# Performance work log

Measured on AMD Instinct MI355X. Metric: run time of the kernel, lower is better.

## Reference

```python
import jax, jax.numpy as jnp
import numpy as np

HOP = 768
NCB = 14
DIM = 512
VOCAB = 1024
W_SCALE = 0.02  # keep conv stacks numerically tame


def conv1d(x, w, b, stride=1, padding=0):
    # x: [B,C,L], w: [O,I,K] (torch layout), b: [O]
    y = jax.lax.conv_general_dilated(
        x, w, window_strides=(stride,), padding=[(padding, padding)],
        dimension_numbers=('NCH', 'OIH', 'NCH'))
    return y + b[None, :, None]


def conv_transpose1d(x, w, b, stride, padding):
    # torch ConvTranspose1d weight layout: (in, out, k)
    k = w.shape[2]
    w2 = jnp.flip(jnp.transpose(w, (1, 0, 2)), axis=2)  # -> OIH
    y = jax.lax.conv_general_dilated(
        x, w2, window_strides=(1,),
        padding=[(k - 1 - padding, k - 1 - padding)],
        lhs_dilation=(stride,),
        dimension_numbers=('NCH', 'OIH', 'NCH'))
    return y + b[None, :, None]


def setup_inputs() -> dict:
    key = jax.random.key(0)
    ks = jax.random.split(key, 16)
    f = lambda k, shp, s=W_SCALE: jax.random.normal(k, shp, dtype=jnp.float32) * s
    B, T = 2, 98304  # T = 768 * 128
    return {
        'audio': jax.random.normal(ks[0], (B, 1, T), dtype=jnp.float32),
        'codebooks': jax.random.normal(ks[1], (NCB, VOCAB, DIM), dtype=jnp.float32),
        'ew1': f(ks[2], (256, 1, 7)), 'eb1': f(ks[3], (256,)),
        'ew2': f(ks[4], (512, 256, 5)), 'eb2': f(ks[5], (512,)),
        'ew3': f(ks[6], (NCB * DIM, 512, 3)), 'eb3': f(ks[7], (NCB * DIM,)),
        'dw1': f(ks[8], (NCB * DIM, 512, 5)), 'db1': f(ks[9], (512,)),
        'dw2': f(ks[10], (256, 512, 5)), 'db2': f(ks[11], (256,)),
        'dw3': f(ks[12], (1, 256, 7)), 'db3': f(ks[13], (1,)),
    }


def reference(audio, codebooks, ew1, eb1, ew2, eb2, ew3, eb3,
              dw1, db1, dw2, db2, dw3, db3):
    B = audio.shape[0]
    # ---- encoder ----
    h = jax.nn.relu(conv1d(audio, ew1, eb1, stride=1, padding=3))
    h = jax.nn.relu(conv1d(h, ew2, eb2, stride=HOP, padding=2))
    h = conv1d(h, ew3, eb3, stride=1, padding=1)          # [B, NCB*DIM, S]
    S = h.shape[-1]
    emb = h.reshape(B, NCB, DIM, S).transpose(0, 1, 3, 2)  # [B, NCB, S, DIM]
    # ---- VQ: per-codebook squared L2 distance + argmin (same argmin as cdist) ----
    d2 = (jnp.sum(emb * emb, axis=-1, keepdims=True)            # [B,NCB,S,1]
          - 2.0 * jnp.einsum('bksd,kvd->bksv', emb, codebooks)  # [B,NCB,S,V]
          + jnp.sum(codebooks * codebooks, axis=-1)[None, :, None, :])
    codes = jnp.argmin(d2, axis=-1)                        # [B, NCB, S] int
    # ---- decode: embedding lookup + transposed conv decoder ----
    q = codebooks[jnp.arange(NCB)[None, :, None], codes]   # [B, NCB, S, DIM]
    q = q.transpose(0, 1, 3, 2).reshape(B, NCB * DIM, S)   # [B, NCB*DIM, S]
    a = jax.nn.relu(conv_transpose1d(q, dw1, db1, stride=HOP, padding=2))
    a = jax.nn.relu(conv1d(a, dw2, db2, stride=1, padding=2))
    a = jnp.tanh(conv1d(a, dw3, db3, stride=1, padding=3))
    return a  # [B, 1, (S-1)*HOP + 1]
```

## Files before the change

### kernel.cpp

```cpp
#include <hip/hip_runtime.h>
#include <hip/hip_bf16.h>
#include <math.h>

#define T_IN 98304
#define SS 128
#define NBATCH 2
#define NN 256
#define C1 256
#define C2 512
#define C3 7168
#define NCBK 14
#define DIMV 512
#define VOC 1024
#define TOUT 97537
#define HOP 768

#define OFF_CBN    0L
#define OFF_AB1    14336L
#define OFF_AB2    14848L
#define OFF_CCONST 15104L
#define OFF_H2C    15120L
#define OFF_H2XH   146192L
#define OFF_H2XL   342800L
#define OFF_H3H    539408L
#define OFF_H3L    1456912L
#define OFF_SCORES 2374416L
#define OFF_X1H    2374416L
#define OFF_X1L    2538256L
#define OFF_DW1T   539408L
#define OFF_XH     539408L
#define OFF_XL     3488528L
#define OFF_CODES  9714448L
#define OFF_QBF    9718032L
#define OFF_A1RAW  10635536L
#define OFF_A2ACT  11290896L

typedef __attribute__((ext_vector_type(8))) short short8;
typedef __attribute__((ext_vector_type(4))) float f32x4;

static __device__ inline ushort f2bf(float x) {
  __hip_bfloat16 h = __float2bfloat16(x);
  return *reinterpret_cast<ushort*>(&h);
}

static __device__ inline void split8(const float4 x0, const float4 x1,
                                     short8& h, short8& l) {
  float xs[8] = {x0.x, x0.y, x0.z, x0.w, x1.x, x1.y, x1.z, x1.w};
  #pragma unroll
  for (int e = 0; e < 8; ++e) {
    uint b = __float_as_uint(xs[e]);
    h[e] = (short)(b >> 16);
    float r = xs[e] - __uint_as_float(b & 0xffff0000u);
    l[e] = (short)(__float_as_uint(r) >> 16);
  }
}

__global__ void k_cbn(const float* __restrict__ cb, float* __restrict__ cbn) {
  int row = blockIdx.x * 4 + (threadIdx.x >> 6);
  int lane = threadIdx.x & 63;
  const float* p = cb + (long)row * DIMV;
  float s = 0.f;
  for (int d = lane; d < DIMV; d += 64) { float x = p[d]; s += x * x; }
  for (int off = 32; off; off >>= 1) s += __shfl_down(s, off);
  if (lane == 0) cbn[row] = s;
}

__global__ __launch_bounds__(256) void k_prep_ab2(const float* __restrict__ db1,
    const float* __restrict__ dw2, const float* __restrict__ db2,
    float* __restrict__ ab1, float* __restrict__ ab2) {
  __shared__ float red[256];
  int o = blockIdx.x, t = threadIdx.x;
  if (o == 0) { ab1[t] = fmaxf(db1[t], 0.f); ab1[t + 256] = fmaxf(db1[t + 256], 0.f); }
  const float* wp = dw2 + (long)o * C2 * 5;
  float acc = 0.f;
  #pragma unroll
  for (int h = 0; h < 2; ++h) {
    int c = t + h * 256;
    const float* p = wp + c * 5;
    float wsum = p[0] + p[1] + p[2] + p[3] + p[4];
    acc = fmaf(wsum, fmaxf(db1[c], 0.f), acc);
  }
  red[t] = acc;
  __syncthreads();
  for (int off = 128; off; off >>= 1) {
    if (t < off) red[t] += red[t + off];
    __syncthreads();
  }
  if (t == 0) ab2[o] = fmaxf(red[0] + db2[o], 0.f);
}

__global__ __launch_bounds__(256) void k_prep_c(const float* __restrict__ dw3,
    const float* __restrict__ db3, const float* __restrict__ ab2,
    float* __restrict__ cconst) {
  __shared__ float red[256];
  int t = threadIdx.x;
  float wsum3 = 0.f;
  #pragma unroll
  for (int j = 0; j < 7; ++j) wsum3 += dw3[t*7+j];
  red[t] = wsum3 * ab2[t];
  __syncthreads();
  for (int off = 128; off; off >>= 1) {
    if (t < off) red[t] += red[t + off];
    __syncthreads();
  }
  if (t == 0) cconst[0] = tanhf(red[0] + db3[0]);
}

__global__ __launch_bounds__(256) void k_enc1(const float* __restrict__ audio,
    const float* __restrict__ ew1, const float* __restrict__ eb1,
    ushort* __restrict__ X1h, ushort* __restrict__ X1l) {
  int n = blockIdx.x, ic = threadIdx.x;
  int b = n >> 7, s = n & 127;
  const float* ap = audio + (long)b * T_IN;
  int base = HOP * s - 5;
  float a[11];
  #pragma unroll
  for (int w = 0; w < 11; ++w) {
    int ai = base + w;
    a[w] = (ai >= 0 && ai < T_IN) ? ap[ai] : 0.f;
  }
  float w1[7];
  #pragma unroll
  for (int j = 0; j < 7; ++j) w1[j] = ew1[ic*7+j];
  float b1 = eb1[ic];
  long off = (long)n * 1280 + ic * 5;
  #pragma unroll
  for (int jj = 0; jj < 5; ++jj) {
    int tcol = HOP * s + jj - 2;
    float v = 0.f;
    if (tcol >= 0) {
      float acc = b1;
      #pragma unroll
      for (int j = 0; j < 7; ++j) acc = fmaf(w1[j], a[jj + j], acc);
      v = fmaxf(acc, 0.f);
    }
    uint bi = __float_as_uint(v);
    X1h[off + jj] = (ushort)(bi >> 16);
    float r = v - __uint_as_float(bi & 0xffff0000u);
    X1l[off + jj] = (ushort)(__float_as_uint(r) >> 16);
  }
}

__global__ __launch_bounds__(256) void gemm_enc2(const float* __restrict__ ew2,
    const ushort* __restrict__ X1h, const ushort* __restrict__ X1l,
    const float* __restrict__ eb2, float* __restrict__ h2c) {
  __shared__ __align__(16) float red[4 * 2048];
  const int tid = threadIdx.x;
  const int w = tid >> 6, lane = tid & 63;
  const int l15 = lane & 15, quad = lane >> 4;
  const int m0 = blockIdx.x * 32, n0 = blockIdx.y * 64;
  const int kbase = w * 320;
  f32x4 acc[2][4] = {};
  const float*  aB = ew2 + (long)(m0 + l15) * 1280 + kbase + quad * 8;
  const ushort* bhB = X1h + (long)(n0 + l15) * 1280 + kbase + quad * 8;
  const ushort* blB = X1l + (long)(n0 + l15) * 1280 + kbase + quad * 8;
  for (int k0 = 0; k0 < 320; k0 += 32) {
    short8 ah[2], al[2], bh[4], bl[4];
    #pragma unroll
    for (int f = 0; f < 2; ++f) {
      const float* ap = aB + (long)f * 16 * 1280 + k0;
      float4 x0 = *(const float4*)ap;
      float4 x1 = *(const float4*)(ap + 4);
      split8(x0, x1, ah[f], al[f]);
    }
    #pragma unroll
    for (int f = 0; f < 4; ++f) {
      bh[f] = *(const short8*)(bhB + (long)f * 16 * 1280 + k0);
      bl[f] = *(const short8*)(blB + (long)f * 16 * 1280 + k0);
    }
    #pragma unroll
    for (int i = 0; i < 2; ++i)
      #pragma unroll
      for (int j = 0; j < 4; ++j) {
        acc[i][j] = __builtin_amdgcn_mfma_f32_16x16x32_bf16(ah[i], bh[j], acc[i][j], 0, 0, 0);
        acc[i][j] = __builtin_amdgcn_mfma_f32_16x16x32_bf16(ah[i], bl[j], acc[i][j], 0, 0, 0);
        acc[i][j] = __builtin_amdgcn_mfma_f32_16x16x32_bf16(al[i], bh[j], acc[i][j], 0, 0, 0);
      }
  }
  #pragma unroll
  for (int i = 0; i < 2; ++i)
    #pragma unroll
    for (int j = 0; j < 4; ++j)
      *(float4*)&red[w * 2048 + (i * 4 + j) * 256 + lane * 4] = *(float4*)&acc[i][j];
  __syncthreads();
  #pragma unroll
  for (int q = 0; q < 2; ++q) {
    const int c = 2 * w + q;
    const int i = c >> 2, j = c & 3;
    float4 s = make_float4(0.f, 0.f, 0.f, 0.f);
    #pragma unroll
    for (int g = 0; g < 4; ++g) {
      float4 t4 = *(const float4*)&red[g * 2048 + c * 256 + lane * 4];
      s.x += t4.x; s.y += t4.y; s.z += t4.z; s.w += t4.w;
    }
    const int obase = m0 + i * 16 + quad * 4;
    float4 bias = *(const float4*)(eb2 + obase);
    const int n = n0 + j * 16 + l15;
    float4 out;
    out.x = fmaxf(s.x + bias.x, 0.f);
    out.y = fmaxf(s.y + bias.y, 0.f);
    out.z = fmaxf(s.z + bias.z, 0.f);
    out.w = fmaxf(s.w + bias.w, 0.f);
    *(float4*)(h2c + (long)n * C2 + obase) = out;
  }
}

__global__ void k_h2x(const float* __restrict__ h2c, ushort* __restrict__ h2xh,
                      ushort* __restrict__ h2xl) {
  int idx = blockIdx.x * 256 + threadIdx.x;
  const int total = NN * 1536;
  for (; idx < total; idx += gridDim.x * 256) {
    int n = idx / 1536, r = idx - n * 1536;
    int ic = r / 3, j = r - ic * 3;
    int s2 = (n & 127) + j - 1;
    int b = n >> 7;
    float v = (s2 >= 0 && s2 < SS) ? h2c[(long)(b*SS + s2)*C2 + ic] : 0.f;
    uint bi = __float_as_uint(v);
    h2xh[idx] = (ushort)(bi >> 16);
    float rr = v - __uint_as_float(bi & 0xffff0000u);
    h2xl[idx] = (ushort)(__float_as_uint(rr) >> 16);
  }
}

__global__ __launch_bounds__(256) void gemm_h3(const float* __restrict__ A,
    const ushort* __restrict__ Bh, const ushort* __restrict__ Bl,
    const float* __restrict__ eb3, ushort* __restrict__ h3h, ushort* __restrict__ h3l) {
  __shared__ __align__(16) float red[4 * 4096];
  const int tid = threadIdx.x;
  const int w = tid >> 6, lane = tid & 63;
  const int l15 = lane & 15, quad = lane >> 4;
  const int m0 = blockIdx.x * 64, n0 = blockIdx.y * 64;
  const int kbase = w * 384;
  f32x4 acc[4][4] = {};
  const float*  aB = A  + (long)(m0 + l15) * 1536 + kbase + quad * 8;
  const ushort* bhB = Bh + (long)(n0 + l15) * 1536 + kbase + quad * 8;
  const ushort* blB = Bl + (long)(n0 + l15) * 1536 + kbase + quad * 8;
  for (int k0 = 0; k0 < 384; k0 += 32) {
    short8 ah[4], al[4], bh[4], bl[4];
    #pragma unroll
    for (int f = 0; f < 4; ++f) {
      const float* ap = aB + (long)f * 16 * 1536 + k0;
      float4 x0 = *(const float4*)ap;
      float4 x1 = *(const float4*)(ap + 4);
      split8(x0, x1, ah[f], al[f]);
      bh[f] = *(const short8*)(bhB + (long)f * 16 * 1536 + k0);
      bl[f] = *(const short8*)(blB + (long)f * 16 * 1536 + k0);
    }
    #pragma unroll
    for (int i = 0; i < 4; ++i)
      #pragma unroll
      for (int j = 0; j < 4; ++j) {
        acc[i][j] = __builtin_amdgcn_mfma_f32_16x16x32_bf16(ah[i], bh[j], acc[i][j], 0, 0, 0);
        acc[i][j] = __builtin_amdgcn_mfma_f32_16x16x32_bf16(ah[i], bl[j], acc[i][j], 0, 0, 0);
        acc[i][j] = __builtin_amdgcn_mfma_f32_16x16x32_bf16(al[i], bh[j], acc[i][j], 0, 0, 0);
      }
  }
  #pragma unroll
  for (int i = 0; i < 4; ++i)
    #pragma unroll
    for (int j = 0; j < 4; ++j)
      *(float4*)&red[w * 4096 + (i * 4 + j) * 256 + lane * 4] = *(float4*)&acc[i][j];
  __syncthreads();
  const int mbase = m0 + w * 16 + quad * 4;
  float4 bias = *(const float4*)(eb3 + mbase);
  #pragma unroll
  for (int j = 0; j < 4; ++j) {
    float4 s = *(const float4*)&red[(w * 4 + j) * 256 + lane * 4];
    #pragma unroll
    for (int r = 1; r < 4; ++r) {
      float4 tt = *(const float4*)&red[r * 4096 + (w * 4 + j) * 256 + lane * 4];
      s.x += tt.x; s.y += tt.y; s.z += tt.z; s.w += tt.w;
    }
    const int n = n0 + j * 16 + l15;
    float v0 = s.x + bias.x;
    float v1 = s.y + bias.y;
    float v2 = s.z + bias.z;
    float v3 = s.w + bias.w;
    uint b0 = __float_as_uint(v0), b1 = __float_as_uint(v1);
    uint b2 = __float_as_uint(v2), b3 = __float_as_uint(v3);
    uint2 hp;
    hp.x = (b0 >> 16) | (b1 & 0xffff0000u);
    hp.y = (b2 >> 16) | (b3 & 0xffff0000u);
    float r0 = v0 - __uint_as_float(b0 & 0xffff0000u);
    float r1 = v1 - __uint_as_float(b1 & 0xffff0000u);
    float r2 = v2 - __uint_as_float(b2 & 0xffff0000u);
    float r3 = v3 - __uint_as_float(b3 & 0xffff0000u);
    uint2 lp;
    lp.x = (__float_as_uint(r0) >> 16) | (__float_as_uint(r1) & 0xffff0000u);
    lp.y = (__float_as_uint(r2) >> 16) | (__float_as_uint(r3) & 0xffff0000u);
    long off = (long)n * C3 + mbase;
    *(uint2*)(h3h + off) = hp;
    *(uint2*)(h3l + off) = lp;
  }
}

__global__ __launch_bounds__(256) void gemm_scores(const float* __restrict__ cb,
    const ushort* __restrict__ h3h, const ushort* __restrict__ h3l,
    const float* __restrict__ cbn, float* __restrict__ scores) {
  __shared__ __align__(16) float red[4 * 4096];
  const int tid = threadIdx.x;
  const int w = tid >> 6, lane = tid & 63;
  const int l15 = lane & 15, quad = lane >> 4;
  const int m0 = blockIdx.x * 64, n0 = blockIdx.y * 64, z = blockIdx.z;
  const int kbase = w * 128;
  f32x4 acc[4][4] = {};
  const float*  aB = cb + (long)z * VOC * DIMV + (long)(m0 + l15) * 512 + kbase + quad * 8;
  const ushort* bhB = h3h + (long)(n0 + l15) * C3 + z * 512 + kbase + quad * 8;
  const ushort* blB = h3l + (long)(n0 + l15) * C3 + z * 512 + kbase + quad * 8;
  for (int k0 = 0; k0 < 128; k0 += 32) {
    short8 ah[4], al[4], bh[4], bl[4];
    #pragma unroll
    for (int f = 0; f < 4; ++f) {
      const float* ap = aB + (long)f * 16 * 512 + k0;
      float4 x0 = *(const float4*)ap;
      float4 x1 = *(const float4*)(ap + 4);
      split8(x0, x1, ah[f], al[f]);
      bh[f] = *(const short8*)(bhB + (long)f * 16 * C3 + k0);
      bl[f] = *(const short8*)(blB + (long)f * 16 * C3 + k0);
    }
    #pragma unroll
    for (int i = 0; i < 4; ++i)
      #pragma unroll
      for (int j = 0; j < 4; ++j) {
        acc[i][j] = __builtin_amdgcn_mfma_f32_16x16x32_bf16(ah[i], bh[j], acc[i][j], 0, 0, 0);
        acc[i][j] = __builtin_amdgcn_mfma_f32_16x16x32_bf16(ah[i], bl[j], acc[i][j], 0, 0, 0);
        acc[i][j] = __builtin_amdgcn_mfma_f32_16x16x32_bf16(al[i], bh[j], acc[i][j], 0, 0, 0);
      }
  }
  #pragma unroll
  for (int i = 0; i < 4; ++i)
    #pragma unroll
    for (int j = 0; j < 4; ++j)
      *(float4*)&red[w * 4096 + (i * 4 + j) * 256 + lane * 4] = *(float4*)&acc[i][j];
  __syncthreads();
  const int vbase = m0 + w * 16 + quad * 4;
  float4 cn = *(const float4*)(cbn + z * VOC + vbase);
  #pragma unroll
  for (int j = 0; j < 4; ++j) {
    float4 s = *(const float4*)&red[(w * 4 + j) * 256 + lane * 4];
    #pragma unroll
    for (int r = 1; r < 4; ++r) {
      float4 tt = *(const float4*)&red[r * 4096 + (w * 4 + j) * 256 + lane * 4];
      s.x += tt.x; s.y += tt.y; s.z += tt.z; s.w += tt.w;
    }
    const int n = n0 + j * 16 + l15;
    float4 out;
    out.x = cn.x - 2.f * s.x;
    out.y = cn.y - 2.f * s.y;
    out.z = cn.z - 2.f * s.z;
    out.w = cn.w - 2.f * s.w;
    *(float4*)(scores + ((long)z * NN + n) * VOC + vbase) = out;
  }
}

__global__ void k_argmin(const float* __restrict__ scores, int* __restrict__ codes) {
  int row = blockIdx.x;
  int lane = threadIdx.x;
  const float* p = scores + (long)row * VOC;
  float best = 3.4e38f; int bi = 0;
  for (int i = 0; i < 16; ++i) {
    int v = i * 64 + lane;
    float x = p[v];
    if (x < best) { best = x; bi = v; }
  }
  for (int off = 32; off; off >>= 1) {
    float ob = __shfl_down(best, off);
    int oi = __shfl_down(bi, off);
    if (ob < best || (ob == best && oi < bi)) { best = ob; bi = oi; }
  }
  if (lane == 0) codes[row] = bi;
}

__global__ __launch_bounds__(256) void k_dw1t(const float* __restrict__ dw1,
                                              ushort* __restrict__ dw1t) {
  __shared__ __align__(16) ushort T[64 * 72];
  int t = threadIdx.x;
  int k0 = blockIdx.x * 64, m0 = blockIdx.y * 64;
  int kk = t >> 2, mj = (t & 3) * 16;
  const float* src = dw1 + (long)(k0 + kk) * 2560 + m0 + mj;
  float x[16];
  *(float4*)&x[0]  = *(const float4*)(src);
  *(float4*)&x[4]  = *(const float4*)(src + 4);
  *(float4*)&x[8]  = *(const float4*)(src + 8);
  *(float4*)&x[12] = *(const float4*)(src + 12);
  #pragma unroll
  for (int l = 0; l < 16; ++l)
    T[(mj + l) * 72 + kk] = f2bf(x[l]);
  __syncthreads();
  int mo = t >> 2, kc = (t & 3) * 16;
  uint4 u0 = *(const uint4*)&T[mo * 72 + kc];
  uint4 u1 = *(const uint4*)&T[mo * 72 + kc + 8];
  ushort* dst = dw1t + (long)(m0 + mo) * C3 + k0 + kc;
  *(uint4*)dst = u0;
  *(uint4*)(dst + 8) = u1;
}

__global__ void k_gather_qbf(const float* __restrict__ cb, const int* __restrict__ codes,
                             ushort* __restrict__ qbf) {
  int idx = blockIdx.x * 256 + threadIdx.x;
  const int total = NN * C3 / 2;
  if (idx >= total) return;
  int n = idx / 3584, rr = idx - n * 3584;
  int k = rr >> 8, dp = rr & 255;
  int code = codes[k * NN + n];
  const float* s = cb + ((long)(k * VOC + code)) * DIMV + dp * 2;
  uint lo = f2bf(s[0]), hi = f2bf(s[1]);
  ((uint*)qbf)[idx] = lo | (hi << 16);
}

__global__ __launch_bounds__(1024) void gemm_a1_mfma(const ushort* __restrict__ dw1t,
    const ushort* __restrict__ qbf, float* __restrict__ a1raw) {
  __shared__ __align__(16) float red[4 * 4096];
  const int tid = threadIdx.x;
  const int w = tid >> 6, lane = tid & 63;
  const int l15 = lane & 15, quad = lane >> 4;
  const int m0 = blockIdx.x * 64, n0 = blockIdx.y * 64;
  const int kbase = w * 448;
  f32x4 acc[4][4] = {};
  const ushort* aB = dw1t + (long)(m0 + l15) * C3 + kbase + quad * 8;
  const ushort* bB = qbf  + (long)(n0 + l15) * C3 + kbase + quad * 8;
  #pragma unroll 2
  for (int k0 = 0; k0 < 448; k0 += 32) {
    short8 ah[4], bh[4];
    #pragma unroll
    for (int f = 0; f < 4; ++f) {
      ah[f] = *(const short8*)(aB + (long)f * 16 * C3 + k0);
      bh[f] = *(const short8*)(bB + (long)f * 16 * C3 + k0);
    }
    #pragma unroll
    for (int i = 0; i < 4; ++i)
      #pragma unroll
      for (int j = 0; j < 4; ++j)
        acc[i][j] = __builtin_amdgcn_mfma_f32_16x16x32_bf16(ah[i], bh[j], acc[i][j], 0, 0, 0);
  }
  float4 rsum = make_float4(0.f, 0.f, 0.f, 0.f);
  #pragma unroll
  for (int r = 0; r < 4; ++r) {
    if ((w >> 2) == r) {
      #pragma unroll
      for (int i = 0; i < 4; ++i)
        #pragma unroll
        for (int j = 0; j < 4; ++j)
          *(float4*)&red[(w & 3) * 4096 + (i * 4 + j) * 256 + lane * 4] = *(float4*)&acc[i][j];
    }
    __syncthreads();
    #pragma unroll
    for (int g = 0; g < 4; ++g) {
      float4 t4 = *(const float4*)&red[g * 4096 + w * 256 + lane * 4];
      rsum.x += t4.x; rsum.y += t4.y; rsum.z += t4.z; rsum.w += t4.w;
    }
    __syncthreads();
  }
  const int ci = w >> 2, cj = w & 3;
  const int n = n0 + cj * 16 + l15;
  const int mb = m0 + ci * 16 + quad * 4;
  float v[4] = {rsum.x, rsum.y, rsum.z, rsum.w};
  #pragma unroll
  for (int reg = 0; reg < 4; ++reg) {
    int m = mb + reg;
    int c = m / 5, jj = m - c * 5;
    a1raw[((long)(n * 5 + jj)) * C2 + c] = v[reg];
  }
}

__global__ void k_x2(const float* __restrict__ a1raw, const float* __restrict__ ab1g,
                     const float* __restrict__ db1, ushort* __restrict__ Xh,
                     ushort* __restrict__ Xl) {
  int idx = blockIdx.x * 256 + threadIdx.x;
  const int total = 2304 * 2560;
  for (; idx < total; idx += gridDim.x * 256) {
    int nu = idx / 2560, ck = idx - nu * 2560;
    int n = nu / 9, u = nu - n * 9;
    int c = ck / 5, jj = ck - c * 5;
    int w = u + jj;
    int s = n & 127;
    int tc = HOP * s - 6 + w;
    float v;
    if (tc < 0 || tc > TOUT - 1) v = 0.f;
    else if (w >= 4 && w <= 8)
      v = fmaxf(db1[c] + a1raw[((long)(n * 5 + (w - 4))) * C2 + c], 0.f);
    else v = ab1g[c];
    uint bi = __float_as_uint(v);
    Xh[idx] = (ushort)(bi >> 16);
    float rr = v - __uint_as_float(bi & 0xffff0000u);
    Xl[idx] = (ushort)(__float_as_uint(rr) >> 16);
  }
}

__global__ __launch_bounds__(256) void gemm_dec2(const float* __restrict__ dw2,
    const ushort* __restrict__ Xh, const ushort* __restrict__ Xl,
    const float* __restrict__ db2, float* __restrict__ a2act) {
  __shared__ __align__(16) float red[4 * 4096];
  const int tid = threadIdx.x;
  const int w = tid >> 6, lane = tid & 63;
  const int l15 = lane & 15, quad = lane >> 4;
  const int m0 = blockIdx.x * 64, n0 = blockIdx.y * 64;
  const int kbase = w * 640;
  f32x4 acc[4][4] = {};
  const float*  aB = dw2 + (long)(m0 + l15) * 2560 + kbase + quad * 8;
  const ushort* bhB = Xh + (long)(n0 + l15) * 2560 + kbase + quad * 8;
  const ushort* blB = Xl + (long)(n0 + l15) * 2560 + kbase + quad * 8;
  for (int k0 = 0; k0 < 640; k0 += 32) {
    short8 ah[4], al[4], bh[4], bl[4];
    #pragma unroll
    for (int f = 0; f < 4; ++f) {
      const float* ap = aB + (long)f * 16 * 2560 + k0;
      float4 x0 = *(const float4*)ap;
      float4 x1 = *(const float4*)(ap + 4);
      split8(x0, x1, ah[f], al[f]);
      bh[f] = *(const short8*)(bhB + (long)f * 16 * 2560 + k0);
      bl[f] = *(const short8*)(blB + (long)f * 16 * 2560 + k0);
    }
    #pragma unroll
    for (int i = 0; i < 4; ++i)
      #pragma unroll
      for (int j = 0; j < 4; ++j) {
        acc[i][j] = __builtin_amdgcn_mfma_f32_16x16x32_bf16(ah[i], bh[j], acc[i][j], 0, 0, 0);
        acc[i][j] = __builtin_amdgcn_mfma_f32_16x16x32_bf16(ah[i], bl[j], acc[i][j], 0, 0, 0);
        acc[i][j] = __builtin_amdgcn_mfma_f32_16x16x32_bf16(al[i], bh[j], acc[i][j], 0, 0, 0);
      }
  }
  #pragma unroll
  for (int i = 0; i < 4; ++i)
    #pragma unroll
    for (int j = 0; j < 4; ++j)
      *(float4*)&red[w * 4096 + (i * 4 + j) * 256 + lane * 4] = *(float4*)&acc[i][j];
  __syncthreads();
  const int mb = m0 + w * 16 + quad * 4;
  float4 bias = *(const float4*)(db2 + mb);
  #pragma unroll
  for (int j = 0; j < 4; ++j) {
    float4 s = *(const float4*)&red[(w * 4 + j) * 256 + lane * 4];
    #pragma unroll
    for (int r = 1; r < 4; ++r) {
      float4 tt = *(const float4*)&red[r * 4096 + (w * 4 + j) * 256 + lane * 4];
      s.x += tt.x; s.y += tt.y; s.z += tt.z; s.w += tt.w;
    }
    const int nu = n0 + j * 16 + l15;
    float4 out;
    out.x = fmaxf(s.x + bias.x, 0.f);
    out.y = fmaxf(s.y + bias.y, 0.f);
    out.z = fmaxf(s.z + bias.z, 0.f);
    out.w = fmaxf(s.w + bias.w, 0.f);
    *(float4*)(a2act + (long)nu * C1 + mb) = out;
  }
}

__global__ void k_fill(float* __restrict__ outp, const float* __restrict__ cconst) {
  float v = cconst[0];
  int idx = blockIdx.x * 256 + threadIdx.x;
  const int total = NBATCH * TOUT;
  for (; idx < total; idx += gridDim.x * 256) outp[idx] = v;
}

__global__ __launch_bounds__(256) void k_dec3(const float* __restrict__ a2act,
    const float* __restrict__ ab2g, const float* __restrict__ dw3,
    const float* __restrict__ db3, float* __restrict__ outp) {
  __shared__ float sa2[9 * C1];
  __shared__ float sb[C1];
  int n = blockIdx.x;
  int s = n & 127, b = n >> 7;
  int t = threadIdx.x;
  for (int i = t; i < 9 * C1; i += 256) sa2[i] = a2act[(long)n * 9 * C1 + i];
  sb[t] = ab2g[t];
  __syncthreads();
  int wv = t >> 6, lane = t & 63;
  float b3 = db3[0];
  for (int w15 = wv; w15 < 15; w15 += 4) {
    int tc = HOP * s - 7 + w15;
    if (tc < 0 || tc > TOUT - 1) continue;
    float part = 0.f;
    for (int cc = lane; cc < C1; cc += 64) {
      #pragma unroll
      for (int j = 0; j < 7; ++j) {
        int wcol = tc + j - 3;
        float x;
        if (wcol < 0 || wcol > TOUT - 1) x = 0.f;
        else {
          int du = wcol - (HOP * s - 4);
          x = (du >= 0 && du <= 8) ? sa2[du * C1 + cc] : sb[cc];
        }
        part = fmaf(dw3[cc*7+j], x, part);
      }
    }
    for (int off = 32; off; off >>= 1) part += __shfl_down(part, off);
    if (lane == 0) outp[(long)b * TOUT + tc] = tanhf(part + b3);
  }
}

extern "C" void kernel_launch(void* const* d_in, const int* in_sizes, int n_in,
                              void* d_out, int out_size, void* d_ws, size_t ws_size,
                              hipStream_t stream) {
  const float* audio = (const float*)d_in[0];
  const float* cb    = (const float*)d_in[1];
  const float* ew1   = (const float*)d_in[2];
  const float* eb1   = (const float*)d_in[3];
  const float* ew2   = (const float*)d_in[4];
  const float* eb2   = (const float*)d_in[5];
  const float* ew3   = (const float*)d_in[6];
  const float* eb3   = (const float*)d_in[7];
  const float* dw1   = (const float*)d_in[8];
  const float* db1   = (const float*)d_in[9];
  const float* dw2   = (const float*)d_in[10];
  const float* db2   = (const float*)d_in[11];
  const float* dw3   = (const float*)d_in[12];
  const float* db3   = (const float*)d_in[13];
  float* outp = (float*)d_out;
  float* ws = (float*)d_ws;

  float*  cbn    = ws + OFF_CBN;
  float*  ab1    = ws + OFF_AB1;
  float*  ab2    = ws + OFF_AB2;
  float*  cconst = ws + OFF_CCONST;
  float*  h2c    = ws + OFF_H2C;
  ushort* h2xh   = (ushort*)(ws + OFF_H2XH);
  ushort* h2xl   = (ushort*)(ws + OFF_H2XL);
  ushort* h3h    = (ushort*)(ws + OFF_H3H);
  ushort* h3l    = (ushort*)(ws + OFF_H3L);
  float*  scores = ws + OFF_SCORES;
  ushort* X1h    = (ushort*)(ws + OFF_X1H);
  ushort* X1l    = (ushort*)(ws + OFF_X1L);
  ushort* dw1t   = (ushort*)(ws + OFF_DW1T);
  ushort* Xh     = (ushort*)(ws + OFF_XH);
  ushort* Xl     = (ushort*)(ws + OFF_XL);
  int*    codes  = (int*)(ws + OFF_CODES);
  ushort* qbf    = (ushort*)(ws + OFF_QBF);
  float*  a1raw  = ws + OFF_A1RAW;
  float*  a2act  = ws + OFF_A2ACT;

  k_cbn<<<3584, 256, 0, stream>>>(cb, cbn);
  k_prep_ab2<<<C1, 256, 0, stream>>>(db1, dw2, db2, ab1, ab2);
  k_prep_c<<<1, 256, 0, stream>>>(dw3, db3, ab2, cconst);
  k_enc1<<<NN, 256, 0, stream>>>(audio, ew1, eb1, X1h, X1l);
  gemm_enc2<<<dim3(16, 4), 256, 0, stream>>>(ew2, X1h, X1l, eb2, h2c);
  k_h2x<<<384, 256, 0, stream>>>(h2c, h2xh, h2xl);
  gemm_h3<<<dim3(112, 4), 256, 0, stream>>>(ew3, h2xh, h2xl, eb3, h3h, h3l);
  gemm_scores<<<dim3(16, 4, 14), 256, 0, stream>>>(cb, h3h, h3l, cbn, scores);
  k_argmin<<<NCBK * NN, 64, 0, stream>>>(scores, codes);
  k_dw1t<<<dim3(112, 40), 256, 0, stream>>>(dw1, dw1t);
  k_gather_qbf<<<3584, 256, 0, stream>>>(cb, codes, qbf);
  gemm_a1_mfma<<<dim3(40, 4), 1024, 0, stream>>>(dw1t, qbf, a1raw);
  k_x2<<<4096, 256, 0, stream>>>(a1raw, ab1, db1, Xh, Xl);
  gemm_dec2<<<dim3(4, 36), 256, 0, stream>>>(dw2, Xh, Xl, db2, a2act);
  k_fill<<<256, 256, 0, stream>>>(outp, cconst);
  k_dec3<<<NN, 256, 0, stream>>>(a2act, ab2, dw3, db3, outp);
}
```

Before: 441.9 us.

## Pre-pack dw1 and gathered codes into MFMA fragment layout for coalesced loads

The dw1 transpose kernel and the codebook gather now write bf16 operands directly in a fragment-tiled layout (16 rows by 32 k per 512-element tile), so each wave's MFMA operand load in gemm_a1 is one contiguous 1 KB read instead of 16 strided row segments. The gather also goes from 2 to 8 elements per thread with float4 reads, cutting its thread count by four. This targets poor coalescing and memory transactions in the decoder's first GEMM and its operand prep, at the cost of more index arithmetic and a layout that only this GEMM understands.

Result: faster. 410.3 us (-7.1%).

```diff
diff --git a/kernel.cpp b/kernel.cpp
--- a/kernel.cpp
+++ b/kernel.cpp
@@ -372,7 +372,7 @@
 }
 
 __global__ __launch_bounds__(256) void k_dw1t(const float* __restrict__ dw1,
-                                              ushort* __restrict__ dw1t) {
+                                              ushort* __restrict__ dw1p) {
   __shared__ __align__(16) ushort T[64 * 72];
   int t = threadIdx.x;
   int k0 = blockIdx.x * 64, m0 = blockIdx.y * 64;
@@ -388,44 +388,60 @@
     T[(mj + l) * 72 + kk] = f2bf(x[l]);
   __syncthreads();
   int mo = t >> 2, kc = (t & 3) * 16;
-  uint4 u0 = *(const uint4*)&T[mo * 72 + kc];
-  uint4 u1 = *(const uint4*)&T[mo * 72 + kc + 8];
-  ushort* dst = dw1t + (long)(m0 + mo) * C3 + k0 + kc;
-  *(uint4*)dst = u0;
-  *(uint4*)(dst + 8) = u1;
+  const int m = m0 + mo;
+  const int mt = m >> 4, l15 = m & 15;
+  #pragma unroll
+  for (int h = 0; h < 2; ++h) {
+    const int kk0 = kc + h * 8;
+    const int kglob = k0 + kk0;
+    const int kt = kglob >> 5;
+    const int quad = (kglob >> 3) & 3;
+    uint4 u = *(const uint4*)&T[mo * 72 + kk0];
+    *(uint4*)(dw1p + ((long)(mt * 224 + kt)) * 512 + (quad * 16 + l15) * 8) = u;
+  }
 }
 
 __global__ void k_gather_qbf(const float* __restrict__ cb, const int* __restrict__ codes,
-                             ushort* __restrict__ qbf) {
-  int idx = blockIdx.x * 256 + threadIdx.x;
-  const int total = NN * C3 / 2;
-  if (idx >= total) return;
-  int n = idx / 3584, rr = idx - n * 3584;
-  int k = rr >> 8, dp = rr & 255;
-  int code = codes[k * NN + n];
-  const float* s = cb + ((long)(k * VOC + code)) * DIMV + dp * 2;
-  uint lo = f2bf(s[0]), hi = f2bf(s[1]);
-  ((uint*)qbf)[idx] = lo | (hi << 16);
-}
-
-__global__ __launch_bounds__(1024) void gemm_a1_mfma(const ushort* __restrict__ dw1t,
-    const ushort* __restrict__ qbf, float* __restrict__ a1raw) {
+                             ushort* __restrict__ qp) {
+  int o = blockIdx.x * 256 + threadIdx.x;
+  const int total = NN * C3 / 8;
+  if (o >= total) return;
+  int frag = o >> 6, r = o & 63;
+  int quad = r >> 4, l15 = r & 15;
+  int nt = frag / 224, kt = frag - nt * 224;
+  int n = nt * 16 + l15;
+  int kglob = kt * 32 + quad * 8;
+  int kcb = kglob >> 9, d0 = kglob & 511;
+  int code = codes[kcb * NN + n];
+  const float* s = cb + ((long)(kcb * VOC + code)) * DIMV + d0;
+  float4 x0 = *(const float4*)s;
+  float4 x1 = *(const float4*)(s + 4);
+  uint4 u;
+  u.x = (uint)f2bf(x0.x) | ((uint)f2bf(x0.y) << 16);
+  u.y = (uint)f2bf(x0.z) | ((uint)f2bf(x0.w) << 16);
+  u.z = (uint)f2bf(x1.x) | ((uint)f2bf(x1.y) << 16);
+  u.w = (uint)f2bf(x1.z) | ((uint)f2bf(x1.w) << 16);
+  ((uint4*)qp)[o] = u;
+}
+
+__global__ __launch_bounds__(1024) void gemm_a1_mfma(const ushort* __restrict__ dw1p,
+    const ushort* __restrict__ qp, float* __restrict__ a1raw) {
   __shared__ __align__(16) float red[4 * 4096];
   const int tid = threadIdx.x;
   const int w = tid >> 6, lane = tid & 63;
   const int l15 = lane & 15, quad = lane >> 4;
-  const int m0 = blockIdx.x * 64, n0 = blockIdx.y * 64;
-  const int kbase = w * 448;
+  const int mt0 = blockIdx.x * 4, nt0 = blockIdx.y * 4;
+  const int kt0 = w * 14;
   f32x4 acc[4][4] = {};
-  const ushort* aB = dw1t + (long)(m0 + l15) * C3 + kbase + quad * 8;
-  const ushort* bB = qbf  + (long)(n0 + l15) * C3 + kbase + quad * 8;
+  const ushort* aB = dw1p + ((long)(mt0 * 224 + kt0)) * 512 + lane * 8;
+  const ushort* bB = qp   + ((long)(nt0 * 224 + kt0)) * 512 + lane * 8;
   #pragma unroll 2
-  for (int k0 = 0; k0 < 448; k0 += 32) {
+  for (int kt = 0; kt < 14; ++kt) {
     short8 ah[4], bh[4];
     #pragma unroll
     for (int f = 0; f < 4; ++f) {
-      ah[f] = *(const short8*)(aB + (long)f * 16 * C3 + k0);
-      bh[f] = *(const short8*)(bB + (long)f * 16 * C3 + k0);
+      ah[f] = *(const short8*)(aB + ((long)(f * 224 + kt)) * 512);
+      bh[f] = *(const short8*)(bB + ((long)(f * 224 + kt)) * 512);
     }
     #pragma unroll
     for (int i = 0; i < 4; ++i)
@@ -452,8 +468,8 @@
     __syncthreads();
   }
   const int ci = w >> 2, cj = w & 3;
-  const int n = n0 + cj * 16 + l15;
-  const int mb = m0 + ci * 16 + quad * 4;
+  const int n = nt0 * 16 + cj * 16 + l15;
+  const int mb = mt0 * 16 + ci * 16 + quad * 4;
   float v[4] = {rsum.x, rsum.y, rsum.z, rsum.w};
   #pragma unroll
   for (int reg = 0; reg < 4; ++reg) {
@@ -620,11 +636,11 @@
   float*  scores = ws + OFF_SCORES;
   ushort* X1h    = (ushort*)(ws + OFF_X1H);
   ushort* X1l    = (ushort*)(ws + OFF_X1L);
-  ushort* dw1t   = (ushort*)(ws + OFF_DW1T);
+  ushort* dw1p   = (ushort*)(ws + OFF_DW1T);
   ushort* Xh     = (ushort*)(ws + OFF_XH);
   ushort* Xl     = (ushort*)(ws + OFF_XL);
   int*    codes  = (int*)(ws + OFF_CODES);
-  ushort* qbf    = (ushort*)(ws + OFF_QBF);
+  ushort* qp     = (ushort*)(ws + OFF_QBF);
   float*  a1raw  = ws + OFF_A1RAW;
   float*  a2act  = ws + OFF_A2ACT;
 
@@ -637,9 +653,9 @@
   gemm_h3<<<dim3(112, 4), 256, 0, stream>>>(ew3, h2xh, h2xl, eb3, h3h, h3l);
   gemm_scores<<<dim3(16, 4, 14), 256, 0, stream>>>(cb, h3h, h3l, cbn, scores);
   k_argmin<<<NCBK * NN, 64, 0, stream>>>(scores, codes);
-  k_dw1t<<<dim3(112, 40), 256, 0, stream>>>(dw1, dw1t);
-  k_gather_qbf<<<3584, 256, 0, stream>>>(cb, codes, qbf);
-  gemm_a1_mfma<<<dim3(40, 4), 1024, 0, stream>>>(dw1t, qbf, a1raw);
+  k_dw1t<<<dim3(112, 40), 256, 0, stream>>>(dw1, dw1p);
+  k_gather_qbf<<<896, 256, 0, stream>>>(cb, codes, qp);
+  gemm_a1_mfma<<<dim3(40, 4), 1024, 0, stream>>>(dw1p, qp, a1raw);
   k_x2<<<4096, 256, 0, stream>>>(a1raw, ab1, db1, Xh, Xl);
   gemm_dec2<<<dim3(4, 36), 256, 0, stream>>>(dw2, Xh, Xl, db2, a2act);
   k_fill<<<256, 256, 0, stream>>>(outp, cconst);
```
